# Kernel tuning notes

Hardware: AMD Instinct MI355X
Metric: run time of the kernel (lower is better)

The kernel has to match this reference:

```python
import jax, jax.numpy as jnp
import numpy as np

D = 1024      # embedding_dimension
F = 4096      # intermediate_dimension
E = 8         # num_experts
K = 2         # top_k
B, S = 4, 2048


def setup_inputs() -> dict:
    key = jax.random.key(0)
    ks = jax.random.split(key, 6)
    scale_in = 1.0 / np.sqrt(D)
    scale_mid = 1.0 / np.sqrt(F)
    return {
        "x": jax.random.normal(ks[0], (B, S, D), dtype=jnp.float32),
        "router_w": jax.random.normal(ks[1], (E, D), dtype=jnp.float32) * scale_in,   # nn.Linear weight [out,in]
        "w1": jax.random.normal(ks[2], (E, F, D), dtype=jnp.float32) * scale_in,
        "b1": jax.random.normal(ks[3], (E, F), dtype=jnp.float32) * 0.01,
        "w2": jax.random.normal(ks[4], (E, D, F), dtype=jnp.float32) * scale_mid,
        "b2": jax.random.normal(ks[5], (E, D), dtype=jnp.float32) * 0.01,
    }


def reference(x, router_w, w1, b1, w2, b2):
    orig_shape = x.shape
    xf = x.reshape(-1, D)                                  # [T, D]
    logits = jnp.einsum("td,ed->te", xf, router_w)        # [T, E]
    top_vals, top_idx = jax.lax.top_k(logits, K)           # [T, K]
    probs = jax.nn.softmax(top_vals, axis=-1)              # [T, K]

    out = jnp.zeros_like(xf)
    for e in range(E):  # small fixed expert loop; masked dense combine
        # combine weight per token for expert e (0 if not routed)
        w = jnp.sum(jnp.where(top_idx == e, probs, 0.0), axis=-1)   # [T]
        h = jax.nn.gelu(jnp.einsum("td,fd->tf", xf, w1[e]) + b1[e], approximate=False)
        y = jnp.einsum("tf,df->td", h, w2[e]) + b2[e]
        out = out + w[:, None] * y
    return out.reshape(orig_shape)
```

## Files before the change

### kernel.cpp

```cpp
#include <hip/hip_runtime.h>
#include <hip/hip_bf16.h>
#include <stdint.h>

#define D 1024
#define F 4096
#define E 8
#define T 8192
#define SLOT_CAP 18432
#define BM 128
#define BK 32
#define EP_STRIDE 136

#define BM2 256
#define BN2 256
#define EP2 264

typedef __attribute__((ext_vector_type(8))) short bf16x8;
typedef __attribute__((ext_vector_type(4))) float f32x4;
typedef __attribute__((ext_vector_type(8))) unsigned short u16x8;

__device__ __forceinline__ unsigned short f2bf(float f) {
  unsigned u = __float_as_uint(f);
  u += 0x7fffu + ((u >> 16) & 1u);
  return (unsigned short)(u >> 16);
}
__device__ __forceinline__ float bf2f(unsigned short u) {
  return __uint_as_float(((unsigned)u) << 16);
}

__device__ __forceinline__ float gelu_f(float v) {
  float s = fabsf(v) * 0.70710678118654752f;
  float t = __builtin_amdgcn_rcpf(fmaf(0.3275911f, s, 1.0f));
  float p = fmaf(t, 1.061405429f, -1.453152027f);
  p = fmaf(t, p, 1.421413741f);
  p = fmaf(t, p, -0.284496736f);
  p = fmaf(t, p, 0.254829592f);
  p = p * t;
  float e = 1.0f - p * __expf(-s * s);
  e = copysignf(e, v);
  return 0.5f * v * (1.0f + e);
}

__device__ __forceinline__ void gload16(const void* g, void* l) {
  auto gp = (const __attribute__((address_space(1))) unsigned int*)(uintptr_t)g;
  auto lp = (__attribute__((address_space(3))) unsigned int*)(unsigned)(uintptr_t)l;
  __builtin_amdgcn_global_load_lds(gp, lp, 16, 0, 0);
}

__global__ __launch_bounds__(256) void prep_kernel(const float* __restrict__ x,
                                                   const float* __restrict__ rw,
                                                   const float* __restrict__ w1,
                                                   int* __restrict__ tok_e,
                                                   float* __restrict__ tok_p,
                                                   unsigned short* __restrict__ xg,
                                                   unsigned short* __restrict__ w1g) {
  if (blockIdx.x >= 2048) {
    int i = (blockIdx.x - 2048) * 256 + threadIdx.x;
    const float4* p = (const float4*)w1 + (size_t)i * 2;
    float4 a = p[0], b = p[1];
    u16x8 o;
    o[0] = f2bf(a.x); o[1] = f2bf(a.y); o[2] = f2bf(a.z); o[3] = f2bf(a.w);
    o[4] = f2bf(b.x); o[5] = f2bf(b.y); o[6] = f2bf(b.z); o[7] = f2bf(b.w);
    *(u16x8*)(w1g + (size_t)i * 8) = o;
    return;
  }
  int t = blockIdx.x * 4 + (threadIdx.x >> 6);
  int lane = threadIdx.x & 63;
  const float* xp = x + (size_t)t * D;
  unsigned short* xgp = xg + (size_t)t * D;
  double acc[E];
#pragma unroll
  for (int e = 0; e < E; e++) acc[e] = 0.0;
  for (int j = 0; j < D / 64; j++) {
    float xv = xp[j * 64 + lane];
    xgp[j * 64 + lane] = f2bf(xv);
#pragma unroll
    for (int e = 0; e < E; e++) acc[e] += (double)xv * (double)rw[e * D + j * 64 + lane];
  }
#pragma unroll
  for (int e = 0; e < E; e++) {
#pragma unroll
    for (int off = 32; off >= 1; off >>= 1) acc[e] += __shfl_xor(acc[e], off, 64);
  }
  if (lane == 0) {
    double v0 = -1e300, v1 = -1e300;
    int i0 = 0, i1 = 0;
#pragma unroll
    for (int e = 0; e < E; e++) {
      double v = acc[e];
      if (v > v0) { v1 = v0; i1 = i0; v0 = v; i0 = e; }
      else if (v > v1) { v1 = v; i1 = e; }
    }
    double e1 = exp(v1 - v0);
    double s = 1.0 + e1;
    tok_e[2 * t] = i0; tok_e[2 * t + 1] = i1;
    tok_p[2 * t] = (float)(1.0 / s);
    tok_p[2 * t + 1] = (float)(e1 / s);
  }
}

__global__ __launch_bounds__(64) void bucket_kernel(const int* __restrict__ tok_e,
                                                    int* __restrict__ perm,
                                                    int* __restrict__ slot_of,
                                                    int* __restrict__ counts,
                                                    int* __restrict__ offp) {
  const int e = blockIdx.x;
  const int lane = threadIdx.x;
  int cnt[E];
#pragma unroll
  for (int ee = 0; ee < E; ee++) cnt[ee] = 0;
  for (int idx = lane; idx < 2 * T; idx += 64) {
    int v = tok_e[idx];
#pragma unroll
    for (int ee = 0; ee < E; ee++) cnt[ee] += (v == ee) ? 1 : 0;
  }
#pragma unroll
  for (int ee = 0; ee < E; ee++) {
#pragma unroll
    for (int off = 32; off >= 1; off >>= 1) cnt[ee] += __shfl_xor(cnt[ee], off, 64);
  }
  int off_e[E + 1];
  int o = 0;
#pragma unroll
  for (int ee = 0; ee < E; ee++) { off_e[ee] = o; o += (cnt[ee] + 255) & ~255; }
  off_e[E] = o;
  if (e == 0 && lane == 0) {
#pragma unroll
    for (int ee = 0; ee < E; ee++) { counts[ee] = cnt[ee]; offp[ee] = off_e[ee]; }
    offp[E] = o;
  }
  int base = 0, mycnt = 0, myend = 0;
#pragma unroll
  for (int ee = 0; ee < E; ee++) {
    if (ee == e) { base = off_e[ee]; mycnt = cnt[ee]; myend = off_e[ee + 1]; }
  }
  const int pad0 = base + mycnt;
  for (int r = 0; r < 2 * T / 64; r++) {
    int idx = r * 64 + lane;
    int v = tok_e[idx];
    bool m = (v == e);
    unsigned long long mask = __ballot(m);
    int pre = __popcll(mask & ((1ull << lane) - 1ull));
    if (m) {
      int slot = base + pre;
      perm[slot] = idx >> 1;
      slot_of[idx] = slot;
    }
    base += __popcll(mask);
  }
  for (int i = pad0 + lane; i < myend; i += 64) perm[i] = 0;
}

__global__ __launch_bounds__(512, 2) void gemm1_kernel(const unsigned short* __restrict__ xg,
                                                       const unsigned short* __restrict__ w1g,
                                                       const float* __restrict__ b1,
                                                       const int* __restrict__ perm,
                                                       const int* __restrict__ offp,
                                                       const int* __restrict__ counts,
                                                       unsigned short* __restrict__ hbuf,
                                                       const float* __restrict__ w2,
                                                       unsigned short* __restrict__ w2g) {
  const int id = blockIdx.x;
  if (id >= 1152) {
    int i = (id - 1152) * 512 + threadIdx.x;
    if (i < E * D * F / 8) {
      const float4* p = (const float4*)w2 + (size_t)i * 2;
      float4 a = p[0], b = p[1];
      u16x8 o;
      o[0] = f2bf(a.x); o[1] = f2bf(a.y); o[2] = f2bf(a.z); o[3] = f2bf(a.w);
      o[4] = f2bf(b.x); o[5] = f2bf(b.y); o[6] = f2bf(b.z); o[7] = f2bf(b.w);
      *(u16x8*)(w2g + (size_t)i * 8) = o;
    }
    return;
  }
  const int swz = (id & 7) * 144 + (id >> 3);
  const int bm = swz >> 4, bn = swz & 15;
  const int row0 = bm * BM2;
  if (row0 >= offp[E]) return;
  int e = 0;
#pragma unroll
  for (int i = 0; i < E; i++) if (row0 >= offp[i + 1]) e = i + 1;
  if (row0 >= offp[e] + counts[e]) return;

  const int t = threadIdx.x, lane = t & 63, w = t >> 6;
  const int wm = w >> 2, wn = w & 3;
  const int fr = lane & 15, fq = lane >> 4;

  __shared__ __align__(16) unsigned short smem[49152];

  const int srow = t >> 2;
  const int c = (t & 3) ^ ((t >> 3) & 3);
  const unsigned short* srcA[2];
  const unsigned short* srcB[2];
  srcA[0] = xg + (size_t)perm[row0 + srow] * D + c * 8;
  srcA[1] = xg + (size_t)perm[row0 + 128 + srow] * D + c * 8;
  srcB[0] = w1g + ((size_t)e * F + (size_t)bn * BN2 + srow) * D + c * 8;
  srcB[1] = w1g + ((size_t)e * F + (size_t)bn * BN2 + 128 + srow) * D + c * 8;

  auto stageA = [&](int tk, int bufi) {
    unsigned short* base = smem + bufi * 16384 + t * 8;
    gload16(srcA[0] + tk * 32, base);
    gload16(srcA[1] + tk * 32, base + 4096);
  };
  auto stageB = [&](int tk, int bufi) {
    unsigned short* base = smem + bufi * 16384 + 8192 + t * 8;
    gload16(srcB[0] + tk * 32, base);
    gload16(srcB[1] + tk * 32, base + 4096);
  };

  int aoff[8], boff[4];
#pragma unroll
  for (int m = 0; m < 8; m++) {
    int row = wm * 128 + m * 16 + fr;
    aoff[m] = row * 32 + ((fq ^ ((row >> 1) & 3)) * 8);
  }
#pragma unroll
  for (int n = 0; n < 4; n++) {
    int row = wn * 64 + n * 16 + fr;
    boff[n] = 8192 + row * 32 + ((fq ^ ((row >> 1) & 3)) * 8);
  }

  f32x4 acc[8][4] = {};

  stageA(0, 0); stageB(0, 0);
  stageA(1, 1); stageB(1, 1);
  asm volatile("s_waitcnt vmcnt(4)" ::: "memory");
  __builtin_amdgcn_s_barrier();
  __builtin_amdgcn_sched_barrier(0);

  const int NK = D / BK;
  int cur = 0, stg = 2;
  for (int kt = 0; kt < NK; ++kt) {
    const unsigned short* tb = smem + cur * 16384;
    bf16x8 a[4], b[4];
#pragma unroll
    for (int m = 0; m < 4; m++) a[m] = *(const bf16x8*)(tb + aoff[m]);
#pragma unroll
    for (int n = 0; n < 4; n++) b[n] = *(const bf16x8*)(tb + boff[n]);
    if (kt + 2 < NK) stageA(kt + 2, stg);
    __builtin_amdgcn_s_barrier();
    asm volatile("s_waitcnt lgkmcnt(0)" ::: "memory");
    __builtin_amdgcn_sched_barrier(0);
    __builtin_amdgcn_s_setprio(1);
#pragma unroll
    for (int m = 0; m < 4; m++)
#pragma unroll
      for (int n = 0; n < 4; n++)
        acc[m][n] = __builtin_amdgcn_mfma_f32_16x16x32_bf16(a[m], b[n], acc[m][n], 0, 0, 0);
    __builtin_amdgcn_s_setprio(0);
    bf16x8 a2[4];
#pragma unroll
    for (int m = 0; m < 4; m++) a2[m] = *(const bf16x8*)(tb + aoff[4 + m]);
    if (kt + 2 < NK) stageB(kt + 2, stg);
    __builtin_amdgcn_s_barrier();
    asm volatile("s_waitcnt lgkmcnt(0)" ::: "memory");
    __builtin_amdgcn_sched_barrier(0);
    __builtin_amdgcn_s_setprio(1);
#pragma unroll
    for (int m = 0; m < 4; m++)
#pragma unroll
      for (int n = 0; n < 4; n++)
        acc[4 + m][n] = __builtin_amdgcn_mfma_f32_16x16x32_bf16(a2[m], b[n], acc[4 + m][n], 0, 0, 0);
    __builtin_amdgcn_s_setprio(0);
    if (kt < NK - 2) { asm volatile("s_waitcnt vmcnt(4)" ::: "memory"); }
    else             { asm volatile("s_waitcnt vmcnt(0)" ::: "memory"); }
    __builtin_amdgcn_s_barrier();
    __builtin_amdgcn_sched_barrier(0);
    cur = (cur == 2) ? 0 : cur + 1;
    stg = (stg == 2) ? 0 : stg + 1;
  }

  float biasv[4];
#pragma unroll
  for (int n = 0; n < 4; n++) biasv[n] = b1[e * F + bn * BN2 + wn * 64 + n * 16 + fr];
  __syncthreads();
#pragma unroll
  for (int p = 0; p < 2; p++) {
    if (wm == p) {
#pragma unroll
      for (int n = 0; n < 4; n++) {
        int col = wn * 64 + n * 16 + fr;
#pragma unroll
        for (int m = 0; m < 8; m++) {
#pragma unroll
          for (int j = 0; j < 4; j++) {
            int lr = m * 16 + fq * 4 + j;
            smem[lr * EP2 + col] = f2bf(gelu_f(acc[m][n][j] + biasv[n]));
          }
        }
      }
    }
    __syncthreads();
#pragma unroll
    for (int i = 0; i < 8; i++) {
      int idx = t + i * 512;
      int r2 = idx >> 5, c8 = (idx & 31) * 8;
      u16x8 v = *(const u16x8*)&smem[r2 * EP2 + c8];
      *(u16x8*)&hbuf[(size_t)(row0 + p * 128 + r2) * F + (size_t)bn * BN2 + c8] = v;
    }
    __syncthreads();
  }
}

__global__ __launch_bounds__(256, 3) void gemm2_kernel(const unsigned short* __restrict__ hbuf,
                                                       const unsigned short* __restrict__ w2g,
                                                       const float* __restrict__ b2,
                                                       const int* __restrict__ offp,
                                                       const int* __restrict__ counts,
                                                       unsigned short* __restrict__ ypart) {
  const int id = blockIdx.x;
  const int swz = (id & 7) * 288 + (id >> 3);
  const int bn = swz & 7;
  const int ks = (swz >> 3) & 1;
  const int bm = swz >> 4;
  const int row0 = bm * BM;
  if (row0 >= offp[E]) return;
  int e = 0;
#pragma unroll
  for (int i = 0; i < E; i++) if (row0 >= offp[i + 1]) e = i + 1;
  const int valid_end = offp[e] + counts[e];
  if (row0 >= valid_end) return;

  const int tid = threadIdx.x, lane = tid & 63, w = tid >> 6;
  __shared__ __align__(16) unsigned short smem[BM * EP_STRIDE];
  unsigned short* As0 = smem;
  unsigned short* Bs0 = smem + 8192;

  const int kbase = ks * (F / 2);
  const unsigned short* gsrc[4];
  unsigned short* ldst[4];
#pragma unroll
  for (int i = 0; i < 4; i++) {
    int ch = tid + 256 * i;
    if (ch < 512) {
      int ar = ch >> 2, ac = (ch & 3) * 8;
      gsrc[i] = hbuf + (size_t)(row0 + ar) * F + kbase + ac;
      ldst[i] = As0 + ch * 8;
    } else {
      int c = ch - 512;
      int br = c >> 2, bc = (c & 3) * 8;
      gsrc[i] = w2g + ((size_t)e * D + (size_t)bn * BM + br) * F + kbase + bc;
      ldst[i] = Bs0 + c * 8;
    }
  }
  auto stage = [&](int k0, int buf) {
#pragma unroll
    for (int i = 0; i < 4; i++) gload16(gsrc[i] + k0, ldst[i] + buf * (BM * BK));
  };

  f32x4 acc[4][4] = {};
  const int wr = (w >> 1) * 64, wc = (w & 1) * 64;
  const int fr = lane & 15, fq = lane >> 4;

  stage(0, 0);
  __syncthreads();
  int cur = 0;
  for (int k0 = 0; k0 < F / 2; k0 += BK) {
    if (k0 + BK < F / 2) stage(k0 + BK, cur ^ 1);
    bf16x8 a[4], b[4];
#pragma unroll
    for (int m = 0; m < 4; m++) a[m] = *(const bf16x8*)&As0[cur * 4096 + (wr + m * 16 + fr) * BK + fq * 8];
#pragma unroll
    for (int n = 0; n < 4; n++) b[n] = *(const bf16x8*)&Bs0[cur * 4096 + (wc + n * 16 + fr) * BK + fq * 8];
#pragma unroll
    for (int m = 0; m < 4; m++)
#pragma unroll
      for (int n = 0; n < 4; n++)
        acc[m][n] = __builtin_amdgcn_mfma_f32_16x16x32_bf16(a[m], b[n], acc[m][n], 0, 0, 0);
    __syncthreads();
    cur ^= 1;
  }

#pragma unroll
  for (int n = 0; n < 4; n++) {
    int cl = wc + n * 16 + fr;
    float bias = (ks == 0) ? b2[e * D + bn * BM + cl] : 0.0f;
#pragma unroll
    for (int m = 0; m < 4; m++) {
#pragma unroll
      for (int j = 0; j < 4; j++) {
        int rl = wr + m * 16 + fq * 4 + j;
        smem[rl * EP_STRIDE + cl] = f2bf(acc[m][n][j] + bias);
      }
    }
  }
  __syncthreads();
  unsigned short* ybase = ypart + (size_t)ks * SLOT_CAP * D;
#pragma unroll
  for (int i = 0; i < 8; i++) {
    int idx = tid + i * 256;
    int r2 = idx >> 4, c = (idx & 15) * 8;
    if (row0 + r2 < valid_end) {
      u16x8 v = *(const u16x8*)&smem[r2 * EP_STRIDE + c];
      *(u16x8*)&ybase[(size_t)(row0 + r2) * D + bn * BM + c] = v;
    }
  }
}

__global__ __launch_bounds__(256) void combine_kernel(const unsigned short* __restrict__ ypart,
                                                      const int* __restrict__ slot_of,
                                                      const float* __restrict__ tok_p,
                                                      float* __restrict__ out) {
  int i = blockIdx.x * 256 + threadIdx.x;
  int t = i >> 7;
  int g8 = i & 127;
  int s0 = slot_of[2 * t], s1 = slot_of[2 * t + 1];
  float g0 = tok_p[2 * t], g1 = tok_p[2 * t + 1];
  const unsigned short* p0 = ypart;
  const unsigned short* p1 = ypart + (size_t)SLOT_CAP * D;
  u16x8 a0 = *(const u16x8*)(p0 + (size_t)s0 * D + g8 * 8);
  u16x8 b0 = *(const u16x8*)(p1 + (size_t)s0 * D + g8 * 8);
  u16x8 a1 = *(const u16x8*)(p0 + (size_t)s1 * D + g8 * 8);
  u16x8 b1 = *(const u16x8*)(p1 + (size_t)s1 * D + g8 * 8);
  float o[8];
#pragma unroll
  for (int j = 0; j < 8; j++)
    o[j] = g0 * (bf2f(a0[j]) + bf2f(b0[j])) + g1 * (bf2f(a1[j]) + bf2f(b1[j]));
  float4* op = (float4*)(out + (size_t)t * D + g8 * 8);
  op[0] = make_float4(o[0], o[1], o[2], o[3]);
  op[1] = make_float4(o[4], o[5], o[6], o[7]);
}

extern "C" void kernel_launch(void* const* d_in, const int* in_sizes, int n_in,
                              void* d_out, int out_size, void* d_ws, size_t ws_size,
                              hipStream_t stream) {
  const float* x = (const float*)d_in[0];
  const float* rw = (const float*)d_in[1];
  const float* w1 = (const float*)d_in[2];
  const float* b1 = (const float*)d_in[3];
  const float* w2 = (const float*)d_in[4];
  const float* b2 = (const float*)d_in[5];
  float* out = (float*)d_out;

  char* ws = (char*)d_ws;
  size_t off = 0;
  auto alloc = [&](size_t bytes) {
    void* p = ws + off;
    off = (off + bytes + 255) & ~(size_t)255;
    return p;
  };
  int* counts = (int*)alloc(E * 4);
  int* offp = (int*)alloc((E + 1) * 4);
  int* tok_e = (int*)alloc((size_t)T * 2 * 4);
  float* tok_p = (float*)alloc((size_t)T * 2 * 4);
  int* perm = (int*)alloc((size_t)SLOT_CAP * 4);
  int* slot_of = (int*)alloc((size_t)T * 2 * 4);
  unsigned short* xg = (unsigned short*)alloc((size_t)T * D * 2);
  unsigned short* w1g = (unsigned short*)alloc((size_t)E * F * D * 2);
  unsigned short* w2g = (unsigned short*)alloc((size_t)E * D * F * 2);
  unsigned short* hbuf = (unsigned short*)alloc((size_t)SLOT_CAP * F * 2);
  unsigned short* ypart = xg;
  (void)ws_size; (void)in_sizes; (void)n_in; (void)out_size;

  hipLaunchKernelGGL(prep_kernel, dim3(2048 + E * F * D / 8 / 256), dim3(256), 0, stream,
                     x, rw, w1, tok_e, tok_p, xg, w1g);
  hipLaunchKernelGGL(bucket_kernel, dim3(E), dim3(64), 0, stream,
                     tok_e, perm, slot_of, counts, offp);
  hipLaunchKernelGGL(gemm1_kernel, dim3(1152 + E * D * F / 8 / 512), dim3(512), 0, stream,
                     xg, w1g, b1, perm, offp, counts, hbuf, w2, w2g);
  hipLaunchKernelGGL(gemm2_kernel, dim3(2304), dim3(256), 0, stream,
                     hbuf, w2g, b2, offp, counts, ypart);
  hipLaunchKernelGGL(combine_kernel, dim3(T * D / 8 / 256), dim3(256), 0, stream,
                     ypart, slot_of, tok_p, out);
}
```

Before: 597.6 us.

## Deepen gemm1 K-tile to 64 with phased pipeline and fold w2 cast into gemm blocks

Raises the gemm1 K-tile from 32 to 64 with double buffering, using an 8-way swizzle and a finer schedule of four sub-phases per tile that interleaves LDS reads, global prefetch of half-tiles, and MFMA groups. The w2 fp32-to-bf16 conversion no longer runs in separate trailing blocks; every gemm1 block, including idle ones, converts part of w2 in a grid-stride loop after its GEMM work. The aim is fewer barriers per unit of K, better overlap of loads with compute, and better use of blocks that have no GEMM rows. In exchange, LDS use grows to 128 KB per block, which may limit occupancy, and busy GEMM blocks now also carry conversion work at their tail.

Result: no change. 604.9 us (+1.2%).

```diff
diff --git a/kernel.cpp b/kernel.cpp
--- a/kernel.cpp
+++ b/kernel.cpp
@@ -10,9 +10,6 @@
 #define BM 128
 #define BK 32
 #define EP_STRIDE 136
-
-#define BM2 256
-#define BN2 256
 #define EP2 264
 
 typedef __attribute__((ext_vector_type(8))) short bf16x8;
@@ -161,144 +158,188 @@
                                                        const float* __restrict__ w2,
                                                        unsigned short* __restrict__ w2g) {
   const int id = blockIdx.x;
-  if (id >= 1152) {
-    int i = (id - 1152) * 512 + threadIdx.x;
-    if (i < E * D * F / 8) {
-      const float4* p = (const float4*)w2 + (size_t)i * 2;
-      float4 a = p[0], b = p[1];
-      u16x8 o;
-      o[0] = f2bf(a.x); o[1] = f2bf(a.y); o[2] = f2bf(a.z); o[3] = f2bf(a.w);
-      o[4] = f2bf(b.x); o[5] = f2bf(b.y); o[6] = f2bf(b.z); o[7] = f2bf(b.w);
-      *(u16x8*)(w2g + (size_t)i * 8) = o;
-    }
-    return;
-  }
   const int swz = (id & 7) * 144 + (id >> 3);
   const int bm = swz >> 4, bn = swz & 15;
-  const int row0 = bm * BM2;
-  if (row0 >= offp[E]) return;
+  const int row0 = bm * 256;
+  const int t = threadIdx.x;
+
+  __shared__ __align__(16) unsigned short smem[65536];
+
+  bool active = (row0 < offp[E]);
   int e = 0;
-#pragma unroll
-  for (int i = 0; i < E; i++) if (row0 >= offp[i + 1]) e = i + 1;
-  if (row0 >= offp[e] + counts[e]) return;
-
-  const int t = threadIdx.x, lane = t & 63, w = t >> 6;
-  const int wm = w >> 2, wn = w & 3;
-  const int fr = lane & 15, fq = lane >> 4;
-
-  __shared__ __align__(16) unsigned short smem[49152];
-
-  const int srow = t >> 2;
-  const int c = (t & 3) ^ ((t >> 3) & 3);
-  const unsigned short* srcA[2];
-  const unsigned short* srcB[2];
-  srcA[0] = xg + (size_t)perm[row0 + srow] * D + c * 8;
-  srcA[1] = xg + (size_t)perm[row0 + 128 + srow] * D + c * 8;
-  srcB[0] = w1g + ((size_t)e * F + (size_t)bn * BN2 + srow) * D + c * 8;
-  srcB[1] = w1g + ((size_t)e * F + (size_t)bn * BN2 + 128 + srow) * D + c * 8;
-
-  auto stageA = [&](int tk, int bufi) {
-    unsigned short* base = smem + bufi * 16384 + t * 8;
-    gload16(srcA[0] + tk * 32, base);
-    gload16(srcA[1] + tk * 32, base + 4096);
-  };
-  auto stageB = [&](int tk, int bufi) {
-    unsigned short* base = smem + bufi * 16384 + 8192 + t * 8;
-    gload16(srcB[0] + tk * 32, base);
-    gload16(srcB[1] + tk * 32, base + 4096);
-  };
-
-  int aoff[8], boff[4];
-#pragma unroll
-  for (int m = 0; m < 8; m++) {
-    int row = wm * 128 + m * 16 + fr;
-    aoff[m] = row * 32 + ((fq ^ ((row >> 1) & 3)) * 8);
-  }
-#pragma unroll
-  for (int n = 0; n < 4; n++) {
-    int row = wn * 64 + n * 16 + fr;
-    boff[n] = 8192 + row * 32 + ((fq ^ ((row >> 1) & 3)) * 8);
-  }
-
-  f32x4 acc[8][4] = {};
-
-  stageA(0, 0); stageB(0, 0);
-  stageA(1, 1); stageB(1, 1);
-  asm volatile("s_waitcnt vmcnt(4)" ::: "memory");
-  __builtin_amdgcn_s_barrier();
-  __builtin_amdgcn_sched_barrier(0);
-
-  const int NK = D / BK;
-  int cur = 0, stg = 2;
-  for (int kt = 0; kt < NK; ++kt) {
-    const unsigned short* tb = smem + cur * 16384;
-    bf16x8 a[4], b[4];
-#pragma unroll
-    for (int m = 0; m < 4; m++) a[m] = *(const bf16x8*)(tb + aoff[m]);
-#pragma unroll
-    for (int n = 0; n < 4; n++) b[n] = *(const bf16x8*)(tb + boff[n]);
-    if (kt + 2 < NK) stageA(kt + 2, stg);
-    __builtin_amdgcn_s_barrier();
-    asm volatile("s_waitcnt lgkmcnt(0)" ::: "memory");
-    __builtin_amdgcn_sched_barrier(0);
-    __builtin_amdgcn_s_setprio(1);
-#pragma unroll
-    for (int m = 0; m < 4; m++)
-#pragma unroll
-      for (int n = 0; n < 4; n++)
-        acc[m][n] = __builtin_amdgcn_mfma_f32_16x16x32_bf16(a[m], b[n], acc[m][n], 0, 0, 0);
-    __builtin_amdgcn_s_setprio(0);
-    bf16x8 a2[4];
-#pragma unroll
-    for (int m = 0; m < 4; m++) a2[m] = *(const bf16x8*)(tb + aoff[4 + m]);
-    if (kt + 2 < NK) stageB(kt + 2, stg);
-    __builtin_amdgcn_s_barrier();
-    asm volatile("s_waitcnt lgkmcnt(0)" ::: "memory");
-    __builtin_amdgcn_sched_barrier(0);
-    __builtin_amdgcn_s_setprio(1);
-#pragma unroll
-    for (int m = 0; m < 4; m++)
-#pragma unroll
-      for (int n = 0; n < 4; n++)
-        acc[4 + m][n] = __builtin_amdgcn_mfma_f32_16x16x32_bf16(a2[m], b[n], acc[4 + m][n], 0, 0, 0);
-    __builtin_amdgcn_s_setprio(0);
-    if (kt < NK - 2) { asm volatile("s_waitcnt vmcnt(4)" ::: "memory"); }
-    else             { asm volatile("s_waitcnt vmcnt(0)" ::: "memory"); }
+  if (active) {
+#pragma unroll
+    for (int i = 0; i < E; i++) if (row0 >= offp[i + 1]) e = i + 1;
+    if (row0 >= offp[e] + counts[e]) active = false;
+  }
+
+  if (active) {
+    const int lane = t & 63, w = t >> 6;
+    const int wm = w >> 2, wn = w & 3;
+    const int fr = lane & 15, fq = lane >> 4;
+
+    const int r0 = t >> 3;
+    const int c0 = (t & 7) ^ (r0 & 7);
+    const unsigned short* pA[4];
+    const unsigned short* pB[4];
+#pragma unroll
+    for (int j = 0; j < 4; j++) {
+      pA[j] = xg + (size_t)perm[row0 + j * 64 + r0] * D + c0 * 8;
+      pB[j] = w1g + ((size_t)e * F + (size_t)bn * 256 + j * 64 + r0) * D + c0 * 8;
+    }
+    auto stgA = [&](int b, int h, int k) {
+      unsigned short* d = smem + b * 32768 + h * 8192 + t * 8;
+      gload16(pA[2 * h] + k, d);
+      gload16(pA[2 * h + 1] + k, d + 4096);
+    };
+    auto stgB = [&](int b, int h, int k) {
+      unsigned short* d = smem + b * 32768 + 16384 + h * 8192 + t * 8;
+      gload16(pB[2 * h] + k, d);
+      gload16(pB[2 * h + 1] + k, d + 4096);
+    };
+
+    int rowA[8], rowB[4];
+#pragma unroll
+    for (int m = 0; m < 8; m++) rowA[m] = (wm * 128 + m * 16 + fr) * 64;
+#pragma unroll
+    for (int n = 0; n < 4; n++) rowB[n] = 16384 + (wn * 64 + n * 16 + fr) * 64;
+    const int sw0 = (fq ^ (fr & 7)) * 8;
+    const int sw1 = ((4 + fq) ^ (fr & 7)) * 8;
+
+    f32x4 acc[8][4] = {};
+    bf16x8 aa[4][2], b1r[2][2], b2r[2][2];
+
+    auto rdA4 = [&](bf16x8 a4[4][2], int mb, int bo) {
+#pragma unroll
+      for (int m = 0; m < 4; m++) {
+        a4[m][0] = *(const bf16x8*)(smem + bo + rowA[mb + m] + sw0);
+        a4[m][1] = *(const bf16x8*)(smem + bo + rowA[mb + m] + sw1);
+      }
+    };
+    auto rdB2 = [&](bf16x8 b2v[2][2], int nb, int bo) {
+#pragma unroll
+      for (int n = 0; n < 2; n++) {
+        b2v[n][0] = *(const bf16x8*)(smem + bo + rowB[nb + n] + sw0);
+        b2v[n][1] = *(const bf16x8*)(smem + bo + rowB[nb + n] + sw1);
+      }
+    };
+    auto mm8 = [&](int mb, int nb, bf16x8 a4[4][2], bf16x8 b2v[2][2]) {
+#pragma unroll
+      for (int m = 0; m < 4; m++)
+#pragma unroll
+        for (int n = 0; n < 2; n++)
+#pragma unroll
+          for (int k = 0; k < 2; k++)
+            acc[mb + m][nb + n] =
+                __builtin_amdgcn_mfma_f32_16x16x32_bf16(a4[m][k], b2v[n][k], acc[mb + m][nb + n], 0, 0, 0);
+    };
+
+#define PH_SYNC() do { \
+    __builtin_amdgcn_s_barrier(); \
+    asm volatile("s_waitcnt lgkmcnt(0)" ::: "memory"); \
+    __builtin_amdgcn_sched_barrier(0); } while (0)
+
+    stgA(0, 0, 0); stgA(0, 1, 0); stgB(0, 0, 0); stgB(0, 1, 0);
+    stgA(1, 0, 64);
+    asm volatile("s_waitcnt vmcnt(2)" ::: "memory");
     __builtin_amdgcn_s_barrier();
     __builtin_amdgcn_sched_barrier(0);
-    cur = (cur == 2) ? 0 : cur + 1;
-    stg = (stg == 2) ? 0 : stg + 1;
-  }
-
-  float biasv[4];
-#pragma unroll
-  for (int n = 0; n < 4; n++) biasv[n] = b1[e * F + bn * BN2 + wn * 64 + n * 16 + fr];
-  __syncthreads();
-#pragma unroll
-  for (int p = 0; p < 2; p++) {
-    if (wm == p) {
-#pragma unroll
-      for (int n = 0; n < 4; n++) {
-        int col = wn * 64 + n * 16 + fr;
-#pragma unroll
-        for (int m = 0; m < 8; m++) {
-#pragma unroll
-          for (int j = 0; j < 4; j++) {
-            int lr = m * 16 + fq * 4 + j;
-            smem[lr * EP2 + col] = f2bf(gelu_f(acc[m][n][j] + biasv[n]));
+
+#pragma unroll 1
+    for (int it = 0; it < 8; ++it) {
+      const int k1 = it * 128 + 64;
+      const int kn0 = it * 128 + 128;
+      const int kn1 = it * 128 + 192;
+      const bool more = (it < 7);
+      rdA4(aa, 0, 0); rdB2(b1r, 0, 0);
+      stgA(1, 1, k1);
+      asm volatile("s_waitcnt lgkmcnt(8)" ::: "memory");
+      PH_SYNC();
+      __builtin_amdgcn_s_setprio(1); mm8(0, 0, aa, b1r); __builtin_amdgcn_s_setprio(0);
+      __builtin_amdgcn_s_barrier();
+      rdB2(b2r, 2, 0);
+      stgB(1, 0, k1);
+      PH_SYNC();
+      __builtin_amdgcn_s_setprio(1); mm8(0, 2, aa, b2r); __builtin_amdgcn_s_setprio(0);
+      __builtin_amdgcn_s_barrier();
+      rdA4(aa, 4, 0);
+      stgB(1, 1, k1);
+      PH_SYNC();
+      __builtin_amdgcn_s_setprio(1); mm8(4, 2, aa, b2r); __builtin_amdgcn_s_setprio(0);
+      __builtin_amdgcn_s_barrier();
+      rdB2(b1r, 0, 0);
+      if (more) stgA(0, 0, kn0);
+      PH_SYNC();
+      __builtin_amdgcn_s_setprio(1); mm8(4, 0, aa, b1r); __builtin_amdgcn_s_setprio(0);
+      if (more) { asm volatile("s_waitcnt vmcnt(2)" ::: "memory"); }
+      else      { asm volatile("s_waitcnt vmcnt(0)" ::: "memory"); }
+      __builtin_amdgcn_s_barrier();
+      rdA4(aa, 0, 32768); rdB2(b1r, 0, 32768);
+      if (more) stgA(0, 1, kn0);
+      asm volatile("s_waitcnt lgkmcnt(8)" ::: "memory");
+      PH_SYNC();
+      __builtin_amdgcn_s_setprio(1); mm8(0, 0, aa, b1r); __builtin_amdgcn_s_setprio(0);
+      __builtin_amdgcn_s_barrier();
+      rdB2(b2r, 2, 32768);
+      if (more) stgB(0, 0, kn0);
+      PH_SYNC();
+      __builtin_amdgcn_s_setprio(1); mm8(0, 2, aa, b2r); __builtin_amdgcn_s_setprio(0);
+      __builtin_amdgcn_s_barrier();
+      rdA4(aa, 4, 32768);
+      if (more) stgB(0, 1, kn0);
+      PH_SYNC();
+      __builtin_amdgcn_s_setprio(1); mm8(4, 2, aa, b2r); __builtin_amdgcn_s_setprio(0);
+      __builtin_amdgcn_s_barrier();
+      rdB2(b1r, 0, 32768);
+      if (more) stgA(1, 0, kn1);
+      PH_SYNC();
+      __builtin_amdgcn_s_setprio(1); mm8(4, 0, aa, b1r); __builtin_amdgcn_s_setprio(0);
+      if (more) { asm volatile("s_waitcnt vmcnt(2)" ::: "memory"); }
+      else      { asm volatile("s_waitcnt vmcnt(0)" ::: "memory"); }
+      __builtin_amdgcn_s_barrier();
+    }
+#undef PH_SYNC
+
+    float biasv[4];
+#pragma unroll
+    for (int n = 0; n < 4; n++) biasv[n] = b1[e * F + bn * 256 + wn * 64 + n * 16 + fr];
+    __syncthreads();
+#pragma unroll
+    for (int p = 0; p < 2; p++) {
+      if (wm == p) {
+#pragma unroll
+        for (int n = 0; n < 4; n++) {
+          int col = wn * 64 + n * 16 + fr;
+#pragma unroll
+          for (int m = 0; m < 8; m++) {
+#pragma unroll
+            for (int j = 0; j < 4; j++) {
+              int lr = m * 16 + fq * 4 + j;
+              smem[lr * EP2 + col] = f2bf(gelu_f(acc[m][n][j] + biasv[n]));
+            }
           }
         }
       }
-    }
-    __syncthreads();
-#pragma unroll
-    for (int i = 0; i < 8; i++) {
-      int idx = t + i * 512;
-      int r2 = idx >> 5, c8 = (idx & 31) * 8;
-      u16x8 v = *(const u16x8*)&smem[r2 * EP2 + c8];
-      *(u16x8*)&hbuf[(size_t)(row0 + p * 128 + r2) * F + (size_t)bn * BN2 + c8] = v;
-    }
-    __syncthreads();
+      __syncthreads();
+#pragma unroll
+      for (int i = 0; i < 8; i++) {
+        int idx = t + i * 512;
+        int r2 = idx >> 5, c8 = (idx & 31) * 8;
+        u16x8 v = *(const u16x8*)&smem[r2 * EP2 + c8];
+        *(u16x8*)&hbuf[(size_t)(row0 + p * 128 + r2) * F + (size_t)bn * 256 + c8] = v;
+      }
+      __syncthreads();
+    }
+  }
+
+  const int total8 = E * D * F / 8;
+  for (int i = id * 512 + t; i < total8; i += 1152 * 512) {
+    const float4* p = (const float4*)w2 + (size_t)i * 2;
+    float4 a = p[0], b = p[1];
+    u16x8 o;
+    o[0] = f2bf(a.x); o[1] = f2bf(a.y); o[2] = f2bf(a.z); o[3] = f2bf(a.w);
+    o[4] = f2bf(b.x); o[5] = f2bf(b.y); o[6] = f2bf(b.z); o[7] = f2bf(b.w);
+    *(u16x8*)(w2g + (size_t)i * 8) = o;
   }
 }
 
@@ -456,7 +497,7 @@
                      x, rw, w1, tok_e, tok_p, xg, w1g);
   hipLaunchKernelGGL(bucket_kernel, dim3(E), dim3(64), 0, stream,
                      tok_e, perm, slot_of, counts, offp);
-  hipLaunchKernelGGL(gemm1_kernel, dim3(1152 + E * D * F / 8 / 512), dim3(512), 0, stream,
+  hipLaunchKernelGGL(gemm1_kernel, dim3(1152), dim3(512), 0, stream,
                      xg, w1g, b1, perm, offp, counts, hbuf, w2, w2g);
   hipLaunchKernelGGL(gemm2_kernel, dim3(2304), dim3(256), 0, stream,
                      hbuf, w2g, b2, offp, counts, ypart);
```
